# Kernel optimization log

Measured on AMD Instinct MI355X. Metric: run time of the kernel, lower is better.

## Reference

```python
import jax, jax.numpy as jnp
import numpy as np

H = 10  # hidden_dim

def _lstm_layer(x_tbd, w_ih, w_hh, b_ih, b_hh):
    # x_tbd: [T, B, D]; w_ih: [4H, D]; w_hh: [4H, H]; biases [4H]
    B = x_tbd.shape[1]
    h0 = jnp.zeros((B, H), x_tbd.dtype)
    c0 = jnp.zeros((B, H), x_tbd.dtype)
    # precompute input projections for all timesteps: [T, B, 4H]
    xg = jnp.einsum('tbd,gd->tbg', x_tbd, w_ih) + b_ih + b_hh

    def step(carry, xg_t):
        h, c = carry
        gates = xg_t + h @ w_hh.T  # [B, 4H]
        i, f, g, o = jnp.split(gates, 4, axis=-1)  # torch gate order i,f,g,o
        i = jax.nn.sigmoid(i); f = jax.nn.sigmoid(f)
        g = jnp.tanh(g); o = jax.nn.sigmoid(o)
        c = f * c + i * g
        h = o * jnp.tanh(c)
        return (h, c), h

    (hT, cT), hs = jax.lax.scan(step, (h0, c0), xg)
    return hs, hT  # hs: [T, B, H]

def setup_inputs() -> dict:
    key = jax.random.key(0)
    ks = jax.random.split(key, 11)
    B, T, D = 32768, 28, 28
    s0 = 1.0 / np.sqrt(H)
    u = lambda k, shape: jax.random.uniform(k, shape, jnp.float32, -s0, s0)
    return {
        'x': jax.random.normal(ks[0], (B, T, D), jnp.float32),
        'w_ih0': u(ks[1], (4 * H, D)),
        'w_hh0': u(ks[2], (4 * H, H)),
        'b_ih0': u(ks[3], (4 * H,)),
        'b_hh0': u(ks[4], (4 * H,)),
        'w_ih1': u(ks[5], (4 * H, H)),
        'w_hh1': u(ks[6], (4 * H, H)),
        'b_ih1': u(ks[7], (4 * H,)),
        'b_hh1': u(ks[8], (4 * H,)),
        'w_cls': u(ks[9], (10, H)),
        'b_cls': u(ks[10], (10,)),
    }

def reference(x, w_ih0, w_hh0, b_ih0, b_hh0, w_ih1, w_hh1, b_ih1, b_hh1, w_cls, b_cls):
    x_tbd = jnp.swapaxes(x, 0, 1)  # [T, B, D]
    hs0, _ = _lstm_layer(x_tbd, w_ih0, w_hh0, b_ih0, b_hh0)
    _, hT1 = _lstm_layer(hs0, w_ih1, w_hh1, b_ih1, b_hh1)  # hT1 = h_n[-1]
    return hT1 @ w_cls.T + b_cls  # [B, 10]
```

## Files before the change

kernel.cpp:

```cpp
#include <hip/hip_runtime.h>


#define HDIM 10
#define DDIM 28
#define TSTEPS 28

typedef __attribute__((ext_vector_type(8))) short short8;
typedef __attribute__((ext_vector_type(4))) float f32x4;

__device__ __forceinline__ unsigned short bf16_rne(float f) {
    unsigned u = __builtin_bit_cast(unsigned, f);
    u += 0x7FFFu + ((u >> 16) & 1u);
    return (unsigned short)(u >> 16);
}
__device__ __forceinline__ float bf16_f(unsigned short h) {
    unsigned u = ((unsigned)h) << 16;
    return __builtin_bit_cast(float, u);
}
__device__ __forceinline__ unsigned pk_hl(float v) {
    unsigned a, p;
    const float z = 0.0f;
    asm("v_cvt_pk_bf16_f32 %0, %1, %2" : "=v"(a) : "v"(v), "v"(z));
    const float hif = __builtin_bit_cast(float, a << 16);
    const float d = v - hif;
    asm("v_cvt_pk_bf16_f32 %0, %1, %2" : "=v"(p) : "v"(v), "v"(d));
    return p;
}
__device__ __forceinline__ float sig_f(float v) {
    return __builtin_amdgcn_rcpf(1.0f + __expf(-v));
}
__device__ __forceinline__ float tanh_f(float v) {
    return 2.0f * __builtin_amdgcn_rcpf(1.0f + __expf(-2.0f * v)) - 1.0f;
}

#define FENCE() __asm volatile("" ::: "memory")
#define WR32(arrp, sidx, val) (*(unsigned*)&(arrp)[(sidx)] = (val))

#define BODY(P, Q, T) do {                                                    \
    _Pragma("unroll")                                                         \
    for (int c = 0; c < 2; ++c)                                               \
        A1f[c] = *(const short8*)&uA1w[lm * 72 + 32 * c + 8 * q];             \
    _Pragma("unroll")                                                         \
    for (int c = 0; c < 4; ++c)                                               \
        A0f[c] = *(const short8*)&uA0w[lm * 136 + 32 * c + 8 * q];            \
    FENCE();                                                                  \
    if ((T) < TSTEPS - 3) {                                                   \
        _Pragma("unroll")                                                     \
        for (int i = 0; i < 7; ++i) { xoff[i] += DDIM; Q[i] = x[xoff[i]]; }   \
    }                                                                         \
    f32x4 C[4], D[4];                                                         \
    _Pragma("unroll")                                                         \
    for (int T4 = 0; T4 < 4; ++T4) {                                          \
        f32x4 accD = {bias1[T4], bias1[T4], bias1[T4], bias1[T4]};            \
        _Pragma("unroll")                                                     \
        for (int c = 0; c < 2; ++c)                                           \
            accD = __builtin_amdgcn_mfma_f32_16x16x32_bf16(A1f[c], B1[T4][c], accD, 0, 0, 0); \
        D[T4] = accD;                                                         \
        f32x4 accC = {bias0[T4], bias0[T4], bias0[T4], bias0[T4]};            \
        _Pragma("unroll")                                                     \
        for (int c = 0; c < 4; ++c)                                           \
            accC = __builtin_amdgcn_mfma_f32_16x16x32_bf16(A0f[c], B0[T4][c], accC, 0, 0, 0); \
        C[T4] = accC;                                                         \
    }                                                                         \
    _Pragma("unroll")                                                         \
    for (int r = 0; r < 4; ++r) {                                             \
        const float i1 = sig_f(D[0][r]);                                      \
        const float f1 = sig_f(D[1][r]);                                      \
        const float g1 = tanh_f(D[2][r]);                                     \
        const float o1 = sig_f(D[3][r]);                                      \
        const float c1 = f1 * c1s[r] + i1 * g1;                               \
        c1s[r] = c1;                                                          \
        h1v[r] = o1 * tanh_f(c1);                                             \
        const float i0 = sig_f(C[0][r]);                                      \
        const float f0 = sig_f(C[1][r]);                                      \
        const float g0 = tanh_f(C[2][r]);                                     \
        const float o0 = sig_f(C[3][r]);                                      \
        const float c0 = f0 * c0s[r] + i0 * g0;                               \
        c0s[r] = c0;                                                          \
        h0v[r] = o0 * tanh_f(c0);                                             \
    }                                                                         \
    if ((T) < TSTEPS - 2) {                                                   \
        _Pragma("unroll")                                                     \
        for (int i = 0; i < 7; ++i) {                                         \
            const unsigned p = pk_hl(P[i]);                                   \
            WR32(uA0w, lofsA[i], p);                                          \
            uA0w[lofsB[i]] = (unsigned short)p;                               \
        }                                                                     \
    }                                                                         \
    if (lm < 10) {                                                            \
        _Pragma("unroll")                                                     \
        for (int r = 0; r < 4; ++r) {                                         \
            const int m = 4 * q + r;                                          \
            const unsigned p1 = pk_hl(h1v[r]);                                \
            unsigned short* r1 = &uA1w[m * 72];                               \
            WR32(r1, 20 + 2 * lm, p1); r1[50 + lm] = (unsigned short)p1;      \
            const unsigned p0 = pk_hl(h0v[r]);                                \
            WR32(r1, 2 * lm, p0);      r1[40 + lm] = (unsigned short)p0;      \
            unsigned short* r0 = &uA0w[m * 136];                              \
            WR32(r0, 56 + 2 * lm, p0); r0[104 + lm] = (unsigned short)p0;     \
        }                                                                     \
    }                                                                         \
    FENCE();                                                                  \
} while (0)

__global__ __launch_bounds__(256) void lstm2_mfma_kernel(
    const float* __restrict__ x,
    const float* __restrict__ w_ih0, const float* __restrict__ w_hh0,
    const float* __restrict__ b_ih0, const float* __restrict__ b_hh0,
    const float* __restrict__ w_ih1, const float* __restrict__ w_hh1,
    const float* __restrict__ b_ih1, const float* __restrict__ b_hh1,
    const float* __restrict__ w_cls, const float* __restrict__ b_cls,
    float* __restrict__ out)
{
    __shared__ __align__(16) unsigned short uA0s[4][16 * 136];
    __shared__ __align__(16) unsigned short uA1s[4][16 * 72];
    __shared__ __align__(16) float hfins[4][16 * 12];

    const int l   = threadIdx.x & 63;
    const int wid = threadIdx.x >> 6;
    const int lm  = l & 15;
    const int q   = l >> 4;
    const int sbase = (blockIdx.x * 4 + wid) * 16;

    unsigned short* const uA0w = uA0s[wid];
    unsigned short* const uA1w = uA1s[wid];
    float* const hfinw = hfins[wid];

    for (int i = l; i < 16 * 22; i += 64) uA0w[(i / 22) * 136 + 114 + (i % 22)] = 0;
    for (int i = l; i < 16 * 12; i += 64) uA1w[(i / 12) * 72 + 60 + (i % 12)] = 0;

    short8 B0[4][4], B1[4][2];
    const bool gvalid = (lm < 10);
    #pragma unroll
    for (int T = 0; T < 4; ++T) {
        const int g = 10 * T + lm;
        #pragma unroll
        for (int c = 0; c < 4; ++c) {
            #pragma unroll
            for (int j = 0; j < 8; ++j) {
                const int kk = 32 * c + 8 * q + j;
                unsigned short bits = 0;
                if (gvalid && kk < 114) {
                    if (kk < 76) {
                        const int j2 = kk >> 1;
                        const float w = (j2 < 28) ? w_ih0[g * 28 + j2]
                                                  : w_hh0[g * 10 + (j2 - 28)];
                        bits = bf16_rne(w);
                    } else {
                        const int d = kk - 76;
                        const float w = (d < 28) ? w_ih0[g * 28 + d]
                                                 : w_hh0[g * 10 + (d - 28)];
                        const unsigned short hi = bf16_rne(w);
                        bits = bf16_rne(w - bf16_f(hi));
                    }
                }
                B0[T][c][j] = (short)bits;
            }
        }
        #pragma unroll
        for (int c = 0; c < 2; ++c) {
            #pragma unroll
            for (int j = 0; j < 8; ++j) {
                const int kk = 32 * c + 8 * q + j;
                unsigned short bits = 0;
                if (gvalid && kk < 60) {
                    if (kk < 40) {
                        const int j2 = kk >> 1;
                        const float w = (j2 < 10) ? w_ih1[g * 10 + j2]
                                                  : w_hh1[g * 10 + (j2 - 10)];
                        bits = bf16_rne(w);
                    } else {
                        const int d = kk - 40;
                        const float w = (d < 10) ? w_ih1[g * 10 + d]
                                                 : w_hh1[g * 10 + (d - 10)];
                        const unsigned short hi = bf16_rne(w);
                        bits = bf16_rne(w - bf16_f(hi));
                    }
                }
                B1[T][c][j] = (short)bits;
            }
        }
    }

    float bias0[4], bias1[4];
    #pragma unroll
    for (int T = 0; T < 4; ++T) {
        const int g = 10 * T + lm;
        bias0[T] = gvalid ? (b_ih0[g] + b_hh0[g]) : 0.0f;
        bias1[T] = gvalid ? (b_ih1[g] + b_hh1[g]) : 0.0f;
    }

    int xoff[7], lofsA[7], lofsB[7];
    float xA[7], xB[7];
    #pragma unroll
    for (int i = 0; i < 7; ++i) {
        const int f = l + 64 * i;
        const int sm = f / 28, d = f - 28 * sm;
        lofsA[i] = sm * 136 + 2 * d;
        lofsB[i] = sm * 136 + 76 + d;
        xoff[i] = (sbase + sm) * (TSTEPS * DDIM) + d;
        xA[i] = x[xoff[i]];
    }
    #pragma unroll
    for (int i = 0; i < 7; ++i) {
        const unsigned p = pk_hl(xA[i]);
        WR32(uA0w, lofsA[i], p);
        uA0w[lofsB[i]] = (unsigned short)p;
    }
    if (lm < 10) {
        #pragma unroll
        for (int r = 0; r < 4; ++r) {
            const int m = 4 * q + r;
            unsigned short* r0 = &uA0w[m * 136];
            WR32(r0, 56 + 2 * lm, 0u); r0[104 + lm] = 0;
            unsigned short* r1 = &uA1w[m * 72];
            WR32(r1, 2 * lm, 0u);      r1[40 + lm] = 0;
            WR32(r1, 20 + 2 * lm, 0u); r1[50 + lm] = 0;
        }
    }
    FENCE();

    float c0s[4] = {0, 0, 0, 0}, c1s[4] = {0, 0, 0, 0};
    float h1v[4] = {0, 0, 0, 0};
    float h0v[4];
    short8 A0f[4], A1f[2];

    #pragma unroll
    for (int i = 0; i < 7; ++i) { xoff[i] += DDIM; xA[i] = x[xoff[i]]; }

    #pragma unroll
    for (int c = 0; c < 4; ++c)
        A0f[c] = *(const short8*)&uA0w[lm * 136 + 32 * c + 8 * q];
    FENCE();
    #pragma unroll
    for (int i = 0; i < 7; ++i) { xoff[i] += DDIM; xB[i] = x[xoff[i]]; }
    {
        f32x4 C[4];
        #pragma unroll
        for (int T = 0; T < 4; ++T) {
            f32x4 acc = {bias0[T], bias0[T], bias0[T], bias0[T]};
            #pragma unroll
            for (int c = 0; c < 4; ++c)
                acc = __builtin_amdgcn_mfma_f32_16x16x32_bf16(A0f[c], B0[T][c], acc, 0, 0, 0);
            C[T] = acc;
        }
        #pragma unroll
        for (int r = 0; r < 4; ++r) {
            const float i0 = sig_f(C[0][r]);
            const float f0 = sig_f(C[1][r]);
            const float g0 = tanh_f(C[2][r]);
            const float o0 = sig_f(C[3][r]);
            const float c0 = f0 * c0s[r] + i0 * g0;
            c0s[r] = c0;
            h0v[r] = o0 * tanh_f(c0);
        }
        if (lm < 10) {
            #pragma unroll
            for (int r = 0; r < 4; ++r) {
                const int m = 4 * q + r;
                const unsigned p0 = pk_hl(h0v[r]);
                unsigned short* r0 = &uA0w[m * 136];
                WR32(r0, 56 + 2 * lm, p0); r0[104 + lm] = (unsigned short)p0;
                unsigned short* r1 = &uA1w[m * 72];
                WR32(r1, 2 * lm, p0);      r1[40 + lm] = (unsigned short)p0;
            }
        }
        #pragma unroll
        for (int i = 0; i < 7; ++i) {
            const unsigned p = pk_hl(xA[i]);
            WR32(uA0w, lofsA[i], p);
            uA0w[lofsB[i]] = (unsigned short)p;
        }
    }
    FENCE();

    #pragma unroll 1
    for (int tp = 0; tp < 13; ++tp) {
        BODY(xB, xA, 2 * tp);
        BODY(xA, xB, 2 * tp + 1);
    }
    BODY(xB, xA, 26);

    {
        #pragma unroll
        for (int c = 0; c < 2; ++c)
            A1f[c] = *(const short8*)&uA1w[lm * 72 + 32 * c + 8 * q];
        FENCE();
        f32x4 D[4];
        #pragma unroll
        for (int T = 0; T < 4; ++T) {
            f32x4 acc = {bias1[T], bias1[T], bias1[T], bias1[T]};
            #pragma unroll
            for (int c = 0; c < 2; ++c)
                acc = __builtin_amdgcn_mfma_f32_16x16x32_bf16(A1f[c], B1[T][c], acc, 0, 0, 0);
            D[T] = acc;
        }
        #pragma unroll
        for (int r = 0; r < 4; ++r) {
            const float i1 = sig_f(D[0][r]);
            const float f1 = sig_f(D[1][r]);
            const float g1 = tanh_f(D[2][r]);
            const float o1 = sig_f(D[3][r]);
            const float c1 = f1 * c1s[r] + i1 * g1;
            h1v[r] = o1 * tanh_f(c1);
        }
    }

    if (lm < 10) {
        #pragma unroll
        for (int r = 0; r < 4; ++r) hfinw[(4 * q + r) * 12 + lm] = h1v[r];
    }
    FENCE();
    if (lm < 10) {
        float wc[10];
        #pragma unroll
        for (int j = 0; j < 10; ++j) wc[j] = w_cls[lm * 10 + j];
        const float bo = b_cls[lm];
        #pragma unroll
        for (int r = 0; r < 4; ++r) {
            const int m = 4 * q + r;
            float acc = bo;
            #pragma unroll
            for (int j = 0; j < 10; ++j) acc += hfinw[m * 12 + j] * wc[j];
            out[(size_t)(sbase + m) * 10 + lm] = acc;
        }
    }
}

extern "C" void kernel_launch(void* const* d_in, const int* in_sizes, int n_in,
                              void* d_out, int out_size, void* d_ws, size_t ws_size,
                              hipStream_t stream) {
    const float* x     = (const float*)d_in[0];
    const float* w_ih0 = (const float*)d_in[1];
    const float* w_hh0 = (const float*)d_in[2];
    const float* b_ih0 = (const float*)d_in[3];
    const float* b_hh0 = (const float*)d_in[4];
    const float* w_ih1 = (const float*)d_in[5];
    const float* w_hh1 = (const float*)d_in[6];
    const float* b_ih1 = (const float*)d_in[7];
    const float* b_hh1 = (const float*)d_in[8];
    const float* w_cls = (const float*)d_in[9];
    const float* b_cls = (const float*)d_in[10];
    float* out = (float*)d_out;

    const int B = in_sizes[0] / (TSTEPS * DDIM);
    const int grid = B / 64;

    hipLaunchKernelGGL(lstm2_mfma_kernel, dim3(grid), dim3(256), 0, stream,
                       x, w_ih0, w_hh0, b_ih0, b_hh0,
                       w_ih1, w_hh1, b_ih1, b_hh1,
                       w_cls, b_cls, out);
}
```

Baseline: 265.8 us.

## Process two 16-row batch tiles per wavefront to interleave independent recurrences

Each wavefront now handles 32 batch samples, as two 16-row MFMA tiles, instead of 16. Blocks shrink to 128 threads (2 waves) so the grid still covers 64 samples per block. The two independent recurrence chains are interleaved in each timestep to hide MFMA and transcendental latency within one wave, and the B-fragment weights are reused across both tiles. In exchange, register pressure roughly doubles, and launch_bounds(128,1) changes the occupancy hint. The total wave count halves, which reduces latency hiding across waves.

```diff
diff --git a/kernel.cpp b/kernel.cpp
--- a/kernel.cpp
+++ b/kernel.cpp
@@ -4,6 +4,7 @@
 #define HDIM 10
 #define DDIM 28
 #define TSTEPS 28
+#define NX 14
 
 typedef __attribute__((ext_vector_type(8))) short short8;
 typedef __attribute__((ext_vector_type(4))) float f32x4;
@@ -38,50 +39,59 @@
 
 #define BODY(P, Q, T) do {                                                    \
     _Pragma("unroll")                                                         \
-    for (int c = 0; c < 2; ++c)                                               \
-        A1f[c] = *(const short8*)&uA1w[lm * 72 + 32 * c + 8 * q];             \
-    _Pragma("unroll")                                                         \
-    for (int c = 0; c < 4; ++c)                                               \
-        A0f[c] = *(const short8*)&uA0w[lm * 136 + 32 * c + 8 * q];            \
+    for (int mh = 0; mh < 2; ++mh) {                                          \
+        _Pragma("unroll")                                                     \
+        for (int c = 0; c < 2; ++c)                                           \
+            A1f[mh][c] = *(const short8*)&uA1w[(16 * mh + lm) * 72 + 32 * c + 8 * q]; \
+        _Pragma("unroll")                                                     \
+        for (int c = 0; c < 4; ++c)                                           \
+            A0f[mh][c] = *(const short8*)&uA0w[(16 * mh + lm) * 136 + 32 * c + 8 * q]; \
+    }                                                                         \
     FENCE();                                                                  \
     if ((T) < TSTEPS - 3) {                                                   \
         _Pragma("unroll")                                                     \
-        for (int i = 0; i < 7; ++i) { xoff[i] += DDIM; Q[i] = x[xoff[i]]; }   \
-    }                                                                         \
-    f32x4 C[4], D[4];                                                         \
+        for (int i = 0; i < NX; ++i) { xoff[i] += DDIM; Q[i] = x[xoff[i]]; }  \
+    }                                                                         \
+    f32x4 C[2][4], D[2][4];                                                   \
     _Pragma("unroll")                                                         \
-    for (int T4 = 0; T4 < 4; ++T4) {                                          \
-        f32x4 accD = {bias1[T4], bias1[T4], bias1[T4], bias1[T4]};            \
-        _Pragma("unroll")                                                     \
-        for (int c = 0; c < 2; ++c)                                           \
-            accD = __builtin_amdgcn_mfma_f32_16x16x32_bf16(A1f[c], B1[T4][c], accD, 0, 0, 0); \
-        D[T4] = accD;                                                         \
-        f32x4 accC = {bias0[T4], bias0[T4], bias0[T4], bias0[T4]};            \
-        _Pragma("unroll")                                                     \
-        for (int c = 0; c < 4; ++c)                                           \
-            accC = __builtin_amdgcn_mfma_f32_16x16x32_bf16(A0f[c], B0[T4][c], accC, 0, 0, 0); \
-        C[T4] = accC;                                                         \
+    for (int mh = 0; mh < 2; ++mh) {                                          \
+        _Pragma("unroll")                                                     \
+        for (int T4 = 0; T4 < 4; ++T4) {                                      \
+            f32x4 accD = {bias1[T4], bias1[T4], bias1[T4], bias1[T4]};        \
+            _Pragma("unroll")                                                 \
+            for (int c = 0; c < 2; ++c)                                       \
+                accD = __builtin_amdgcn_mfma_f32_16x16x32_bf16(A1f[mh][c], B1[T4][c], accD, 0, 0, 0); \
+            D[mh][T4] = accD;                                                 \
+            f32x4 accC = {bias0[T4], bias0[T4], bias0[T4], bias0[T4]};        \
+            _Pragma("unroll")                                                 \
+            for (int c = 0; c < 4; ++c)                                       \
+                accC = __builtin_amdgcn_mfma_f32_16x16x32_bf16(A0f[mh][c], B0[T4][c], accC, 0, 0, 0); \
+            C[mh][T4] = accC;                                                 \
+        }                                                                     \
     }                                                                         \
     _Pragma("unroll")                                                         \
-    for (int r = 0; r < 4; ++r) {                                             \
-        const float i1 = sig_f(D[0][r]);                                      \
-        const float f1 = sig_f(D[1][r]);                                      \
-        const float g1 = tanh_f(D[2][r]);                                     \
-        const float o1 = sig_f(D[3][r]);                                      \
-        const float c1 = f1 * c1s[r] + i1 * g1;                               \
-        c1s[r] = c1;                                                          \
-        h1v[r] = o1 * tanh_f(c1);                                             \
-        const float i0 = sig_f(C[0][r]);                                      \
-        const float f0 = sig_f(C[1][r]);                                      \
-        const float g0 = tanh_f(C[2][r]);                                     \
-        const float o0 = sig_f(C[3][r]);                                      \
-        const float c0 = f0 * c0s[r] + i0 * g0;                               \
-        c0s[r] = c0;                                                          \
-        h0v[r] = o0 * tanh_f(c0);                                             \
+    for (int mh = 0; mh < 2; ++mh) {                                          \
+        _Pragma("unroll")                                                     \
+        for (int r = 0; r < 4; ++r) {                                         \
+            const float i1 = sig_f(D[mh][0][r]);                              \
+            const float f1 = sig_f(D[mh][1][r]);                              \
+            const float g1 = tanh_f(D[mh][2][r]);                             \
+            const float o1 = sig_f(D[mh][3][r]);                              \
+            const float c1 = f1 * c1s[mh][r] + i1 * g1;                       \
+            c1s[mh][r] = c1;                                                  \
+            h1v[mh][r] = o1 * tanh_f(c1);                                     \
+            const float i0 = sig_f(C[mh][0][r]);                              \
+            const float f0 = sig_f(C[mh][1][r]);                              \
+            const float g0 = tanh_f(C[mh][2][r]);                             \
+            const float o0 = sig_f(C[mh][3][r]);                              \
+            const float c0 = f0 * c0s[mh][r] + i0 * g0;                       \
+            c0s[mh][r] = c0;                                                  \
+            h0v[mh][r] = o0 * tanh_f(c0);                                     \
+        }                                                                     \
     }                                                                         \
     if ((T) < TSTEPS - 2) {                                                   \
         _Pragma("unroll")                                                     \
-        for (int i = 0; i < 7; ++i) {                                         \
+        for (int i = 0; i < NX; ++i) {                                        \
             const unsigned p = pk_hl(P[i]);                                   \
             WR32(uA0w, lofsA[i], p);                                          \
             uA0w[lofsB[i]] = (unsigned short)p;                               \
@@ -89,21 +99,24 @@
     }                                                                         \
     if (lm < 10) {                                                            \
         _Pragma("unroll")                                                     \
-        for (int r = 0; r < 4; ++r) {                                         \
-            const int m = 4 * q + r;                                          \
-            const unsigned p1 = pk_hl(h1v[r]);                                \
-            unsigned short* r1 = &uA1w[m * 72];                               \
-            WR32(r1, 20 + 2 * lm, p1); r1[50 + lm] = (unsigned short)p1;      \
-            const unsigned p0 = pk_hl(h0v[r]);                                \
-            WR32(r1, 2 * lm, p0);      r1[40 + lm] = (unsigned short)p0;      \
-            unsigned short* r0 = &uA0w[m * 136];                              \
-            WR32(r0, 56 + 2 * lm, p0); r0[104 + lm] = (unsigned short)p0;     \
+        for (int mh = 0; mh < 2; ++mh) {                                      \
+            _Pragma("unroll")                                                 \
+            for (int r = 0; r < 4; ++r) {                                     \
+                const int m = 16 * mh + 4 * q + r;                            \
+                const unsigned p1 = pk_hl(h1v[mh][r]);                        \
+                unsigned short* r1 = &uA1w[m * 72];                           \
+                WR32(r1, 20 + 2 * lm, p1); r1[50 + lm] = (unsigned short)p1;  \
+                const unsigned p0 = pk_hl(h0v[mh][r]);                        \
+                WR32(r1, 2 * lm, p0);      r1[40 + lm] = (unsigned short)p0;  \
+                unsigned short* r0 = &uA0w[m * 136];                          \
+                WR32(r0, 56 + 2 * lm, p0); r0[104 + lm] = (unsigned short)p0; \
+            }                                                                 \
         }                                                                     \
     }                                                                         \
     FENCE();                                                                  \
 } while (0)
 
-__global__ __launch_bounds__(256) void lstm2_mfma_kernel(
+__global__ __launch_bounds__(128, 1) void lstm2_mfma_kernel(
     const float* __restrict__ x,
     const float* __restrict__ w_ih0, const float* __restrict__ w_hh0,
     const float* __restrict__ b_ih0, const float* __restrict__ b_hh0,
@@ -112,22 +125,22 @@
     const float* __restrict__ w_cls, const float* __restrict__ b_cls,
     float* __restrict__ out)
 {
-    __shared__ __align__(16) unsigned short uA0s[4][16 * 136];
-    __shared__ __align__(16) unsigned short uA1s[4][16 * 72];
-    __shared__ __align__(16) float hfins[4][16 * 12];
+    __shared__ __align__(16) unsigned short uA0s[2][32 * 136];
+    __shared__ __align__(16) unsigned short uA1s[2][32 * 72];
+    __shared__ __align__(16) float hfins[2][32 * 12];
 
     const int l   = threadIdx.x & 63;
     const int wid = threadIdx.x >> 6;
     const int lm  = l & 15;
     const int q   = l >> 4;
-    const int sbase = (blockIdx.x * 4 + wid) * 16;
+    const int sbase = (blockIdx.x * 2 + wid) * 32;
 
     unsigned short* const uA0w = uA0s[wid];
     unsigned short* const uA1w = uA1s[wid];
     float* const hfinw = hfins[wid];
 
-    for (int i = l; i < 16 * 22; i += 64) uA0w[(i / 22) * 136 + 114 + (i % 22)] = 0;
-    for (int i = l; i < 16 * 12; i += 64) uA1w[(i / 12) * 72 + 60 + (i % 12)] = 0;
+    for (int i = l; i < 32 * 22; i += 64) uA0w[(i / 22) * 136 + 114 + (i % 22)] = 0;
+    for (int i = l; i < 32 * 12; i += 64) uA1w[(i / 12) * 72 + 60 + (i % 12)] = 0;
 
     short8 B0[4][4], B1[4][2];
     const bool gvalid = (lm < 10);
@@ -190,10 +203,10 @@
         bias1[T] = gvalid ? (b_ih1[g] + b_hh1[g]) : 0.0f;
     }
 
-    int xoff[7], lofsA[7], lofsB[7];
-    float xA[7], xB[7];
-    #pragma unroll
-    for (int i = 0; i < 7; ++i) {
+    int xoff[NX], lofsA[NX], lofsB[NX];
+    float xA[NX], xB[NX];
+    #pragma unroll
+    for (int i = 0; i < NX; ++i) {
         const int f = l + 64 * i;
         const int sm = f / 28, d = f - 28 * sm;
         lofsA[i] = sm * 136 + 2 * d;
@@ -202,71 +215,85 @@
         xA[i] = x[xoff[i]];
     }
     #pragma unroll
-    for (int i = 0; i < 7; ++i) {
+    for (int i = 0; i < NX; ++i) {
         const unsigned p = pk_hl(xA[i]);
         WR32(uA0w, lofsA[i], p);
         uA0w[lofsB[i]] = (unsigned short)p;
     }
     if (lm < 10) {
         #pragma unroll
-        for (int r = 0; r < 4; ++r) {
-            const int m = 4 * q + r;
-            unsigned short* r0 = &uA0w[m * 136];
-            WR32(r0, 56 + 2 * lm, 0u); r0[104 + lm] = 0;
-            unsigned short* r1 = &uA1w[m * 72];
-            WR32(r1, 2 * lm, 0u);      r1[40 + lm] = 0;
-            WR32(r1, 20 + 2 * lm, 0u); r1[50 + lm] = 0;
+        for (int mh = 0; mh < 2; ++mh) {
+            #pragma unroll
+            for (int r = 0; r < 4; ++r) {
+                const int m = 16 * mh + 4 * q + r;
+                unsigned short* r0 = &uA0w[m * 136];
+                WR32(r0, 56 + 2 * lm, 0u); r0[104 + lm] = 0;
+                unsigned short* r1 = &uA1w[m * 72];
+                WR32(r1, 2 * lm, 0u);      r1[40 + lm] = 0;
+                WR32(r1, 20 + 2 * lm, 0u); r1[50 + lm] = 0;
+            }
         }
     }
     FENCE();
 
-    float c0s[4] = {0, 0, 0, 0}, c1s[4] = {0, 0, 0, 0};
-    float h1v[4] = {0, 0, 0, 0};
-    float h0v[4];
-    short8 A0f[4], A1f[2];
-
-    #pragma unroll
-    for (int i = 0; i < 7; ++i) { xoff[i] += DDIM; xA[i] = x[xoff[i]]; }
-
-    #pragma unroll
-    for (int c = 0; c < 4; ++c)
-        A0f[c] = *(const short8*)&uA0w[lm * 136 + 32 * c + 8 * q];
+    float c0s[2][4] = {{0,0,0,0},{0,0,0,0}}, c1s[2][4] = {{0,0,0,0},{0,0,0,0}};
+    float h1v[2][4] = {{0,0,0,0},{0,0,0,0}};
+    float h0v[2][4];
+    short8 A0f[2][4], A1f[2][2];
+
+    #pragma unroll
+    for (int i = 0; i < NX; ++i) { xoff[i] += DDIM; xA[i] = x[xoff[i]]; }
+
+    #pragma unroll
+    for (int mh = 0; mh < 2; ++mh)
+        #pragma unroll
+        for (int c = 0; c < 4; ++c)
+            A0f[mh][c] = *(const short8*)&uA0w[(16 * mh + lm) * 136 + 32 * c + 8 * q];
     FENCE();
     #pragma unroll
-    for (int i = 0; i < 7; ++i) { xoff[i] += DDIM; xB[i] = x[xoff[i]]; }
+    for (int i = 0; i < NX; ++i) { xoff[i] += DDIM; xB[i] = x[xoff[i]]; }
     {
-        f32x4 C[4];
-        #pragma unroll
-        for (int T = 0; T < 4; ++T) {
-            f32x4 acc = {bias0[T], bias0[T], bias0[T], bias0[T]};
-            #pragma unroll
-            for (int c = 0; c < 4; ++c)
-                acc = __builtin_amdgcn_mfma_f32_16x16x32_bf16(A0f[c], B0[T][c], acc, 0, 0, 0);
-            C[T] = acc;
-        }
-        #pragma unroll
-        for (int r = 0; r < 4; ++r) {
-            const float i0 = sig_f(C[0][r]);
-            const float f0 = sig_f(C[1][r]);
-            const float g0 = tanh_f(C[2][r]);
-            const float o0 = sig_f(C[3][r]);
-            const float c0 = f0 * c0s[r] + i0 * g0;
-            c0s[r] = c0;
-            h0v[r] = o0 * tanh_f(c0);
+        f32x4 C[2][4];
+        #pragma unroll
+        for (int mh = 0; mh < 2; ++mh) {
+            #pragma unroll
+            for (int T = 0; T < 4; ++T) {
+                f32x4 acc = {bias0[T], bias0[T], bias0[T], bias0[T]};
+                #pragma unroll
+                for (int c = 0; c < 4; ++c)
+                    acc = __builtin_amdgcn_mfma_f32_16x16x32_bf16(A0f[mh][c], B0[T][c], acc, 0, 0, 0);
+                C[mh][T] = acc;
+            }
+        }
+        #pragma unroll
+        for (int mh = 0; mh < 2; ++mh) {
+            #pragma unroll
+            for (int r = 0; r < 4; ++r) {
+                const float i0 = sig_f(C[mh][0][r]);
+                const float f0 = sig_f(C[mh][1][r]);
+                const float g0 = tanh_f(C[mh][2][r]);
+                const float o0 = sig_f(C[mh][3][r]);
+                const float c0 = f0 * c0s[mh][r] + i0 * g0;
+                c0s[mh][r] = c0;
+                h0v[mh][r] = o0 * tanh_f(c0);
+            }
         }
         if (lm < 10) {
             #pragma unroll
-            for (int r = 0; r < 4; ++r) {
-                const int m = 4 * q + r;
-                const unsigned p0 = pk_hl(h0v[r]);
-                unsigned short* r0 = &uA0w[m * 136];
-                WR32(r0, 56 + 2 * lm, p0); r0[104 + lm] = (unsigned short)p0;
-                unsigned short* r1 = &uA1w[m * 72];
-                WR32(r1, 2 * lm, p0);      r1[40 + lm] = (unsigned short)p0;
-            }
-        }
-        #pragma unroll
-        for (int i = 0; i < 7; ++i) {
+            for (int mh = 0; mh < 2; ++mh) {
+                #pragma unroll
+                for (int r = 0; r < 4; ++r) {
+                    const int m = 16 * mh + 4 * q + r;
+                    const unsigned p0 = pk_hl(h0v[mh][r]);
+                    unsigned short* r0 = &uA0w[m * 136];
+                    WR32(r0, 56 + 2 * lm, p0); r0[104 + lm] = (unsigned short)p0;
+                    unsigned short* r1 = &uA1w[m * 72];
+                    WR32(r1, 2 * lm, p0);      r1[40 + lm] = (unsigned short)p0;
+                }
+            }
+        }
+        #pragma unroll
+        for (int i = 0; i < NX; ++i) {
             const unsigned p = pk_hl(xA[i]);
             WR32(uA0w, lofsA[i], p);
             uA0w[lofsB[i]] = (unsigned short)p;
@@ -283,32 +310,43 @@
 
     {
         #pragma unroll
-        for (int c = 0; c < 2; ++c)
-            A1f[c] = *(const short8*)&uA1w[lm * 72 + 32 * c + 8 * q];
+        for (int mh = 0; mh < 2; ++mh)
+            #pragma unroll
+            for (int c = 0; c < 2; ++c)
+                A1f[mh][c] = *(const short8*)&uA1w[(16 * mh + lm) * 72 + 32 * c + 8 * q];
         FENCE();
-        f32x4 D[4];
-        #pragma unroll
-        for (int T = 0; T < 4; ++T) {
-            f32x4 acc = {bias1[T], bias1[T], bias1[T], bias1[T]};
-            #pragma unroll
-            for (int c = 0; c < 2; ++c)
-                acc = __builtin_amdgcn_mfma_f32_16x16x32_bf16(A1f[c], B1[T][c], acc, 0, 0, 0);
-            D[T] = acc;
-        }
-        #pragma unroll
-        for (int r = 0; r < 4; ++r) {
-            const float i1 = sig_f(D[0][r]);
-            const float f1 = sig_f(D[1][r]);
-            const float g1 = tanh_f(D[2][r]);
-            const float o1 = sig_f(D[3][r]);
-            const float c1 = f1 * c1s[r] + i1 * g1;
-            h1v[r] = o1 * tanh_f(c1);
+        f32x4 D[2][4];
+        #pragma unroll
+        for (int mh = 0; mh < 2; ++mh) {
+            #pragma unroll
+            for (int T = 0; T < 4; ++T) {
+                f32x4 acc = {bias1[T], bias1[T], bias1[T], bias1[T]};
+                #pragma unroll
+                for (int c = 0; c < 2; ++c)
+                    acc = __builtin_amdgcn_mfma_f32_16x16x32_bf16(A1f[mh][c], B1[T][c], acc, 0, 0, 0);
+                D[mh][T] = acc;
+            }
+        }
+        #pragma unroll
+        for (int mh = 0; mh < 2; ++mh) {
+            #pragma unroll
+            for (int r = 0; r < 4; ++r) {
+                const float i1 = sig_f(D[mh][0][r]);
+                const float f1 = sig_f(D[mh][1][r]);
+                const float g1 = tanh_f(D[mh][2][r]);
+                const float o1 = sig_f(D[mh][3][r]);
+                const float c1 = f1 * c1s[mh][r] + i1 * g1;
+                h1v[mh][r] = o1 * tanh_f(c1);
+            }
         }
     }
 
     if (lm < 10) {
         #pragma unroll
-        for (int r = 0; r < 4; ++r) hfinw[(4 * q + r) * 12 + lm] = h1v[r];
+        for (int mh = 0; mh < 2; ++mh)
+            #pragma unroll
+            for (int r = 0; r < 4; ++r)
+                hfinw[(16 * mh + 4 * q + r) * 12 + lm] = h1v[mh][r];
     }
     FENCE();
     if (lm < 10) {
@@ -317,12 +355,15 @@
         for (int j = 0; j < 10; ++j) wc[j] = w_cls[lm * 10 + j];
         const float bo = b_cls[lm];
         #pragma unroll
-        for (int r = 0; r < 4; ++r) {
-            const int m = 4 * q + r;
-            float acc = bo;
-            #pragma unroll
-            for (int j = 0; j < 10; ++j) acc += hfinw[m * 12 + j] * wc[j];
-            out[(size_t)(sbase + m) * 10 + lm] = acc;
+        for (int mh = 0; mh < 2; ++mh) {
+            #pragma unroll
+            for (int r = 0; r < 4; ++r) {
+                const int m = 16 * mh + 4 * q + r;
+                float acc = bo;
+                #pragma unroll
+                for (int j = 0; j < 10; ++j) acc += hfinw[m * 12 + j] * wc[j];
+                out[(size_t)(sbase + m) * 10 + lm] = acc;
+            }
         }
     }
 }
@@ -346,7 +387,7 @@
     const int B = in_sizes[0] / (TSTEPS * DDIM);
     const int grid = B / 64;
 
-    hipLaunchKernelGGL(lstm2_mfma_kernel, dim3(grid), dim3(256), 0, stream,
+    hipLaunchKernelGGL(lstm2_mfma_kernel, dim3(grid), dim3(128), 0, stream,
                        x, w_ih0, w_hh0, b_ih0, b_hh0,
                        w_ih1, w_hh1, b_ih1, b_hh1,
                        w_cls, b_cls, out);
```

Result: faster. 232.9 us (-12.4%).
